# Optimization experiments

Hardware: AMD Instinct MI355X
Metric: run time of the kernel (lower is better)

Reference implementation:

```python
import jax, jax.numpy as jnp
import numpy as np

B, S, H = 2, 2048, 2048
NH = 16
Q_LORA = 1536
KV_LORA = 512
NOPE = 128
ROPE = 64
QHD = NOPE + ROPE  # 192
VHD = 128
FF = 8192
EPS = 1e-6
THETA = 10000.0


def rmsnorm(x, w, eps=EPS):
    var = jnp.mean(jnp.square(x), axis=-1, keepdims=True)
    return w * (x * jax.lax.rsqrt(var + eps))


def rotate_half(x):
    x1 = x[..., : x.shape[-1] // 2]
    x2 = x[..., x.shape[-1] // 2 :]
    return jnp.concatenate((-x2, x1), axis=-1)


def _deinterleave(x):
    # torch: x.view(b,h,s,d//2,2).transpose(0,1,2,4,3).reshape(b,h,s,d)
    b, h, s, d = x.shape
    return x.reshape(b, h, s, d // 2, 2).transpose(0, 1, 2, 4, 3).reshape(b, h, s, d)


def setup_inputs() -> dict:
    key = jax.random.key(0)
    ks = jax.random.split(key, 16)
    sc = 0.02
    # RoPE tables [S, ROPE]
    inv_freq = 1.0 / (THETA ** (np.arange(0, ROPE, 2, dtype=np.float64) / ROPE))
    freqs = np.outer(np.arange(S, dtype=np.float64), inv_freq)
    emb = np.concatenate([freqs, freqs], axis=-1)
    pos = jnp.sort(jax.random.randint(ks[15], (B, S), 0, S), axis=-1)
    return {
        "hidden_states": jax.random.normal(ks[0], (B, S, H), jnp.float32),
        "ln1_w": jnp.ones((H,), jnp.float32),
        "q_a_kernel": jax.random.normal(ks[1], (H, Q_LORA), jnp.float32) * sc,
        "q_a_ln_w": jnp.ones((Q_LORA,), jnp.float32),
        "q_b_kernel": jax.random.normal(ks[2], (Q_LORA, NH * QHD), jnp.float32) * sc,
        "kv_a_kernel": jax.random.normal(ks[3], (H, KV_LORA + ROPE), jnp.float32) * sc,
        "kv_a_ln_w": jnp.ones((KV_LORA,), jnp.float32),
        "kv_b_kernel": jax.random.normal(ks[4], (KV_LORA, NH * (NOPE + VHD)), jnp.float32) * sc,
        "o_kernel": jax.random.normal(ks[5], (NH * VHD, H), jnp.float32) * sc,
        "ln2_w": jnp.ones((H,), jnp.float32),
        "gate_kernel": jax.random.normal(ks[6], (H, FF), jnp.float32) * sc,
        "up_kernel": jax.random.normal(ks[7], (H, FF), jnp.float32) * sc,
        "down_kernel": jax.random.normal(ks[8], (FF, H), jnp.float32) * sc,
        "sin": jnp.asarray(np.sin(emb), jnp.float32),
        "cos": jnp.asarray(np.cos(emb), jnp.float32),
        "position_ids": pos,
    }


def reference(hidden_states, ln1_w, q_a_kernel, q_a_ln_w, q_b_kernel,
              kv_a_kernel, kv_a_ln_w, kv_b_kernel, o_kernel, ln2_w,
              gate_kernel, up_kernel, down_kernel, sin, cos, position_ids):
    b, s, h = hidden_states.shape
    x = rmsnorm(hidden_states, ln1_w)

    # --- MLA attention ---
    q = rmsnorm(x @ q_a_kernel, q_a_ln_w) @ q_b_kernel        # [b,s,NH*QHD]
    q = q.reshape(b, s, NH, QHD).transpose(0, 2, 1, 3)        # [b,NH,s,QHD]
    q_nope, q_pe = q[..., :NOPE], q[..., NOPE:]

    ckv = x @ kv_a_kernel                                     # [b,s,KV_LORA+ROPE]
    k_pe = ckv[..., KV_LORA:].reshape(b, s, 1, ROPE).transpose(0, 2, 1, 3)  # [b,1,s,ROPE]
    kv = rmsnorm(ckv[..., :KV_LORA], kv_a_ln_w) @ kv_b_kernel
    kv = kv.reshape(b, s, NH, NOPE + VHD).transpose(0, 2, 1, 3)
    k_nope = kv[..., :NOPE]
    v = kv[..., NOPE:]                                        # [b,NH,s,VHD]

    cos_e = cos[position_ids][:, None]                        # [b,1,s,ROPE]
    sin_e = sin[position_ids][:, None]
    q_pe = _deinterleave(q_pe)
    k_pe = _deinterleave(k_pe)
    q_pe = q_pe * cos_e + rotate_half(q_pe) * sin_e
    k_pe = k_pe * cos_e + rotate_half(k_pe) * sin_e

    qs = jnp.concatenate([q_nope, q_pe], axis=-1)             # [b,NH,s,QHD]
    ks = jnp.concatenate([k_nope, jnp.broadcast_to(k_pe, (b, NH, s, ROPE))], axis=-1)

    scale = QHD ** -0.5
    scores = jnp.einsum("bhqd,bhkd->bhqk", qs, ks) * scale
    causal = jnp.tril(jnp.ones((s, s), dtype=bool))
    scores = jnp.where(causal, scores, jnp.finfo(scores.dtype).min)
    probs = jax.nn.softmax(scores, axis=-1)
    attn = jnp.einsum("bhqk,bhkd->bhqd", probs, v)            # [b,NH,s,VHD]
    attn = attn.transpose(0, 2, 1, 3).reshape(b, s, NH * VHD)
    attn_out = attn @ o_kernel

    h1 = hidden_states + attn_out

    # --- dense MLP (SwiGLU) ---
    x2 = rmsnorm(h1, ln2_w)
    mlp = (jax.nn.silu(x2 @ gate_kernel) * (x2 @ up_kernel)) @ down_kernel
    return h1 + mlp
```

## Files before the change

kernel.cpp:

```cpp
#include <hip/hip_runtime.h>
#include <hip/hip_bf16.h>
#include <cstdint>

#define B_ 2
#define S_ 2048
#define H_ 2048
#define NH_ 16
#define QL_ 1536
#define KVL_ 512
#define NOPE_ 128
#define ROPE_ 64
#define QHD_ 192
#define VHD_ 128
#define FF_ 8192
#define BS_ (B_ * S_)
#define CKVP_ 640
#define KVW_ (NOPE_ + VHD_)

typedef __hip_bfloat16 bf16;
typedef __attribute__((ext_vector_type(8))) short short8_t;
typedef __attribute__((ext_vector_type(4))) float f32x4;

__device__ __forceinline__ float ldf(const float* p, size_t i) { return p[i]; }
__device__ __forceinline__ float ldf(const bf16* p, size_t i) { return __bfloat162float(p[i]); }
__device__ __forceinline__ void stf(float* p, size_t i, float v) { p[i] = v; }
__device__ __forceinline__ void stf(bf16* p, size_t i, float v) { p[i] = __float2bfloat16(v); }

__device__ __forceinline__ void gload16(const void* g, void* l)
{
    __builtin_amdgcn_global_load_lds((const unsigned int*)g, (unsigned int*)l, 16, 0, 0);
}

__global__ __launch_bounds__(256) void transp_bf16(
    const float* __restrict__ in, bf16* __restrict__ out, int K, int N, int Npad)
{
    __shared__ float t[32][33];
    const int n0 = blockIdx.x * 32, k0 = blockIdx.y * 32;
    for (int r = threadIdx.y; r < 32; r += 8) {
        const int n = n0 + threadIdx.x;
        t[r][threadIdx.x] = (n < N) ? in[(size_t)(k0 + r) * N + n] : 0.f;
    }
    __syncthreads();
    for (int r = threadIdx.y; r < 32; r += 8) {
        out[(size_t)(n0 + r) * K + k0 + threadIdx.x] = __float2bfloat16(t[threadIdx.x][r]);
    }
}

template<typename InT, typename OutT>
__global__ __launch_bounds__(256) void rmsnorm2(
    const InT* __restrict__ in, const float* __restrict__ w,
    OutT* __restrict__ out, int cols, int istride, int ostride)
{
    const int row = blockIdx.x;
    const InT* ip = in + (size_t)row * istride;
    OutT* op = out + (size_t)row * ostride;

    float ss = 0.f;
    for (int c = threadIdx.x; c < cols; c += 256) {
        float v = ldf(ip, c);
        ss = fmaf(v, v, ss);
    }
    #pragma unroll
    for (int off = 32; off; off >>= 1) ss += __shfl_xor(ss, off);
    __shared__ float red[4];
    if ((threadIdx.x & 63) == 0) red[threadIdx.x >> 6] = ss;
    __syncthreads();
    const float total = red[0] + red[1] + red[2] + red[3];
    const float scale = rsqrtf(total / (float)cols + 1e-6f);
    for (int c = threadIdx.x; c < cols; c += 256) {
        stf(op, c, ldf(ip, c) * scale * w[c]);
    }
}

template<int MODE, typename OutT>
__global__ __launch_bounds__(256) void gemm_bf16(
    const bf16* __restrict__ A, const bf16* __restrict__ BT,
    const float* __restrict__ Df, const bf16* __restrict__ Db,
    OutT* __restrict__ C, int M, int N, int K)
{
    __shared__ short As[128 * 32];
    __shared__ short Bs[128 * 32];
    const int tid = threadIdx.x;
    const int wid = tid >> 6, lane = tid & 63;
    const int bm = blockIdx.y * 128, bn = blockIdx.x * 128;
    const int wr = (wid >> 1) * 64, wc = (wid & 1) * 64;
    const int l16 = lane & 15;
    const int lk = (lane >> 4) << 3;

    f32x4 acc[4][4] = {};

    for (int k0 = 0; k0 < K; k0 += 32) {
        #pragma unroll
        for (int is = 0; is < 2; ++is) {
            const int c = is * 256 + tid;
            const int row = c >> 2;
            const int cb = (c & 3) * 16;
            const char* srcA = (const char*)A + ((size_t)(bm + row) * K + k0) * 2 + cb;
            const char* srcB = (const char*)BT + ((size_t)(bn + row) * K + k0) * 2 + cb;
            char* dstA = (char*)As + (is * 256 + wid * 64) * 16;
            char* dstB = (char*)Bs + (is * 256 + wid * 64) * 16;
            gload16(srcA, dstA);
            gload16(srcB, dstB);
        }
        __syncthreads();

        short8_t a[4], b[4];
        const short* ApW = As + (wr + l16) * 32 + lk;
        const short* BpW = Bs + (wc + l16) * 32 + lk;
        #pragma unroll
        for (int m = 0; m < 4; ++m) a[m] = *(const short8_t*)(ApW + m * 16 * 32);
        #pragma unroll
        for (int n = 0; n < 4; ++n) b[n] = *(const short8_t*)(BpW + n * 16 * 32);
        #pragma unroll
        for (int m = 0; m < 4; ++m)
            #pragma unroll
            for (int n = 0; n < 4; ++n)
                acc[m][n] = __builtin_amdgcn_mfma_f32_16x16x32_bf16(a[m], b[n], acc[m][n], 0, 0, 0);
        __syncthreads();
    }

    const int r0 = bm + wr + ((lane >> 4) << 2);
    const int c0 = bn + wc + l16;
    #pragma unroll
    for (int m = 0; m < 4; ++m) {
        #pragma unroll
        for (int n = 0; n < 4; ++n) {
            const int row = r0 + m * 16;
            const int col = c0 + n * 16;
            #pragma unroll
            for (int r = 0; r < 4; ++r) {
                const size_t off = (size_t)(row + r) * N + col;
                float v = acc[m][n][r];
                if (MODE == 1) v += Df[off];
                if (MODE == 2) {
                    const float g = __bfloat162float(Db[off]);
                    v *= g / (1.f + __expf(-g));
                }
                stf(C, off, v);
            }
        }
    }
}

__device__ __forceinline__ short8_t ldsfrag(const short* half_base, int r, int c)
{
    return *(const short8_t*)(half_base + r * 64 + ((c ^ (r & 7)) << 3));
}

template<int MODE, typename OutT>
__global__ __launch_bounds__(512, 2) void gemm256(
    const bf16* __restrict__ A, const bf16* __restrict__ BT,
    const float* __restrict__ Df, const bf16* __restrict__ Db,
    OutT* __restrict__ C, int M, int N, int K)
{
    __shared__ short lds[2][2][2][128 * 64];

    const int tid = threadIdx.x;
    const int wid = tid >> 6, lane = tid & 63;
    const int wm = wid >> 2, wn = wid & 3;
    const int l16 = lane & 15, hk = lane >> 4;

    const int nwg = gridDim.x * gridDim.y;
    const int orig = blockIdx.y * gridDim.x + blockIdx.x;
    const int q = nwg >> 3, r8 = nwg & 7;
    const int xcd = orig & 7, lid = orig >> 3;
    const int wg = (xcd < r8 ? xcd * (q + 1) : r8 * (q + 1) + (xcd - r8) * q) + lid;
    const int bn = (wg % gridDim.x) * 256;
    const int bm = (wg / gridDim.x) * 256;

    f32x4 acc[8][4] = {};

    const int nt = K >> 6;

    auto stage_half = [&](const bf16* gbase, int ldk, short* lbase) {
        #pragma unroll
        for (int i = 0; i < 2; ++i) {
            const int ch = i * 512 + tid;
            const int row = ch >> 3, pc = ch & 7;
            const int gc = pc ^ (row & 7);
            const char* src = (const char*)(gbase + (size_t)row * ldk + gc * 8);
            char* dst = (char*)lbase + (i * 512 + wid * 64) * 16;
            gload16(src, dst);
        }
    };

    stage_half(A + (size_t)bm * K, K, &lds[0][0][0][0]);
    stage_half(A + (size_t)(bm + 128) * K, K, &lds[0][0][1][0]);
    stage_half(BT + (size_t)bn * K, K, &lds[0][1][0][0]);
    stage_half(BT + (size_t)(bn + 128) * K, K, &lds[0][1][1][0]);
    asm volatile("s_waitcnt vmcnt(0)" ::: "memory");
    __syncthreads();

    int cur = 0;
    for (int t = 0; t < nt; ++t) {
        const int k0n = (t + 1) << 6;
        const short* Ah = &lds[cur][0][wm][0];
        const short* Bh = &lds[cur][1][wn >> 1][0];
        const int brr = (wn & 1) * 64;

        short8_t bfr[4][2], afr[2][2];

        #pragma unroll
        for (int nf = 0; nf < 4; ++nf)
            #pragma unroll
            for (int ks = 0; ks < 2; ++ks)
                bfr[nf][ks] = ldsfrag(Bh, brr + nf * 16 + l16, ks * 4 + hk);
        #pragma unroll
        for (int mi = 0; mi < 2; ++mi)
            #pragma unroll
            for (int ks = 0; ks < 2; ++ks)
                afr[mi][ks] = ldsfrag(Ah, mi * 16 + l16, ks * 4 + hk);
        if (t + 1 < nt) {
            stage_half(A + (size_t)bm * K + k0n, K, &lds[cur ^ 1][0][0][0]);
            stage_half(A + (size_t)(bm + 128) * K + k0n, K, &lds[cur ^ 1][0][1][0]);
        }
        __builtin_amdgcn_s_barrier();
        __builtin_amdgcn_s_setprio(1);
        #pragma unroll
        for (int mi = 0; mi < 2; ++mi)
            #pragma unroll
            for (int nf = 0; nf < 4; ++nf)
                #pragma unroll
                for (int ks = 0; ks < 2; ++ks)
                    acc[mi][nf] = __builtin_amdgcn_mfma_f32_16x16x32_bf16(
                        afr[mi][ks], bfr[nf][ks], acc[mi][nf], 0, 0, 0);
        __builtin_amdgcn_s_setprio(0);
        __builtin_amdgcn_s_barrier();

        #pragma unroll
        for (int mi = 0; mi < 2; ++mi)
            #pragma unroll
            for (int ks = 0; ks < 2; ++ks)
                afr[mi][ks] = ldsfrag(Ah, 32 + mi * 16 + l16, ks * 4 + hk);
        if (t + 1 < nt) {
            stage_half(BT + (size_t)bn * K + k0n, K, &lds[cur ^ 1][1][0][0]);
            stage_half(BT + (size_t)(bn + 128) * K + k0n, K, &lds[cur ^ 1][1][1][0]);
        }
        __builtin_amdgcn_s_barrier();
        __builtin_amdgcn_s_setprio(1);
        #pragma unroll
        for (int mi = 0; mi < 2; ++mi)
            #pragma unroll
            for (int nf = 0; nf < 4; ++nf)
                #pragma unroll
                for (int ks = 0; ks < 2; ++ks)
                    acc[2 + mi][nf] = __builtin_amdgcn_mfma_f32_16x16x32_bf16(
                        afr[mi][ks], bfr[nf][ks], acc[2 + mi][nf], 0, 0, 0);
        __builtin_amdgcn_s_setprio(0);
        __builtin_amdgcn_s_barrier();

        #pragma unroll
        for (int mi = 0; mi < 2; ++mi)
            #pragma unroll
            for (int ks = 0; ks < 2; ++ks)
                afr[mi][ks] = ldsfrag(Ah, 64 + mi * 16 + l16, ks * 4 + hk);
        __builtin_amdgcn_s_barrier();
        __builtin_amdgcn_s_setprio(1);
        #pragma unroll
        for (int mi = 0; mi < 2; ++mi)
            #pragma unroll
            for (int nf = 0; nf < 4; ++nf)
                #pragma unroll
                for (int ks = 0; ks < 2; ++ks)
                    acc[4 + mi][nf] = __builtin_amdgcn_mfma_f32_16x16x32_bf16(
                        afr[mi][ks], bfr[nf][ks], acc[4 + mi][nf], 0, 0, 0);
        __builtin_amdgcn_s_setprio(0);
        __builtin_amdgcn_s_barrier();

        #pragma unroll
        for (int mi = 0; mi < 2; ++mi)
            #pragma unroll
            for (int ks = 0; ks < 2; ++ks)
                afr[mi][ks] = ldsfrag(Ah, 96 + mi * 16 + l16, ks * 4 + hk);
        __builtin_amdgcn_s_barrier();
        __builtin_amdgcn_s_setprio(1);
        #pragma unroll
        for (int mi = 0; mi < 2; ++mi)
            #pragma unroll
            for (int nf = 0; nf < 4; ++nf)
                #pragma unroll
                for (int ks = 0; ks < 2; ++ks)
                    acc[6 + mi][nf] = __builtin_amdgcn_mfma_f32_16x16x32_bf16(
                        afr[mi][ks], bfr[nf][ks], acc[6 + mi][nf], 0, 0, 0);
        __builtin_amdgcn_s_setprio(0);
        asm volatile("s_waitcnt vmcnt(0)" ::: "memory");
        __syncthreads();
        cur ^= 1;
    }

    const int r0 = bm + wm * 128 + (lane >> 4) * 4;
    const int c0 = bn + wn * 64 + l16;
    #pragma unroll
    for (int mf = 0; mf < 8; ++mf) {
        #pragma unroll
        for (int nf = 0; nf < 4; ++nf) {
            const int row = r0 + mf * 16;
            const int col = c0 + nf * 16;
            #pragma unroll
            for (int r = 0; r < 4; ++r) {
                const size_t off = (size_t)(row + r) * N + col;
                float v = acc[mf][nf][r];
                if (MODE == 1) v += Df[off];
                if (MODE == 2) {
                    const float g = __bfloat162float(Db[off]);
                    v *= g / (1.f + __expf(-g));
                }
                stf(C, off, v);
            }
        }
    }
}

__global__ __launch_bounds__(256) void rope_kernel(
    bf16* __restrict__ q, float* __restrict__ ckv,
    const int* __restrict__ pos_ids,
    const float* __restrict__ sinT, const float* __restrict__ cosT)
{
    const int wid = blockIdx.x * 4 + (threadIdx.x >> 6);
    const int lane = threadIdx.x & 63;
    const int NQ = BS_ * NH_;

    int bs;
    bf16* bptr = nullptr;
    float* fptr = nullptr;
    if (wid < NQ) {
        bs = wid >> 4;
        bptr = q + (size_t)wid * QHD_ + NOPE_;
    } else {
        bs = wid - NQ;
        fptr = ckv + (size_t)bs * CKVP_ + KVL_;
    }
    const int pos = pos_ids[bs];
    const float c  = cosT[pos * ROPE_ + lane];
    const float sn = sinT[pos * ROPE_ + lane];
    const float x = bptr ? __bfloat162float(bptr[lane]) : fptr[lane];
    const int j = lane & 31;
    const float x0 = __shfl(x, 2 * j);
    const float x1 = __shfl(x, 2 * j + 1);
    const float res = (lane < 32) ? fmaf(x0, c, -x1 * sn) : fmaf(x1, c, x0 * sn);
    if (bptr) bptr[lane] = __float2bfloat16(res);
    else      fptr[lane] = res;
}

__global__ __launch_bounds__(256) void pack_k(
    const float* __restrict__ KV, const float* __restrict__ CKV,
    bf16* __restrict__ Kh)
{
    const int total = BS_ * NH_ * (QHD_ / 2);
    for (int i = blockIdx.x * 256 + threadIdx.x; i < total; i += gridDim.x * 256) {
        const int d2 = i % (QHD_ / 2);
        const int t  = i / (QHD_ / 2);
        const int s  = t % S_;
        const int hh = (t / S_) % NH_;
        const int bb = t / (S_ * NH_);
        const int d = d2 * 2;
        float2 v;
        if (d < NOPE_) v = *(const float2*)&KV[(((size_t)bb * S_ + s) * NH_ + hh) * KVW_ + d];
        else           v = *(const float2*)&CKV[((size_t)bb * S_ + s) * CKVP_ + KVL_ + (d - NOPE_)];
        union { bf16 h[2]; unsigned int u; } cv;
        cv.h[0] = __float2bfloat16(v.x);
        cv.h[1] = __float2bfloat16(v.y);
        *(unsigned int*)&Kh[((size_t)(bb * NH_ + hh) * S_ + s) * QHD_ + d] = cv.u;
    }
}

__global__ __launch_bounds__(256) void pack_vt(
    const float* __restrict__ KV, bf16* __restrict__ Vt)
{
    __shared__ float t[32][33];
    const int s0 = blockIdx.x * 32, d0 = blockIdx.y * 32;
    const int bh = blockIdx.z;
    const int tx = threadIdx.x & 31, ty = threadIdx.x >> 5;
    for (int r = ty; r < 32; r += 8)
        t[r][tx] = KV[(((size_t)(bh >> 4) * S_ + s0 + r) * NH_ + (bh & 15)) * KVW_ + NOPE_ + d0 + tx];
    __syncthreads();
    for (int r = ty; r < 32; r += 8)
        Vt[((size_t)bh * VHD_ + d0 + r) * S_ + s0 + tx] = __float2bfloat16(t[tx][r]);
}

__global__ __launch_bounds__(512, 2) void attn_mfma(
    const bf16* __restrict__ Qp, const bf16* __restrict__ Kh,
    const bf16* __restrict__ Vt, bf16* __restrict__ outp)
{
    __shared__ __align__(16) short Ks[64][192];
    __shared__ __align__(16) short Vs[128][64];
    __shared__ __align__(16) short Ps[8][16][64];

    const int tid = threadIdx.x;
    const int wid = tid >> 6, lane = tid & 63;
    const int l16 = lane & 15;
    const int hk  = lane >> 4;
    const int lk  = hk << 3;
    const int pr  = hk << 2;
    const int lx  = l16 & 7;

    const int bid = blockIdx.x;
    const int orig = (bid & 7) * 64 + (bid >> 3);
    const int j  = orig & 15;
    const int gh = orig >> 4;
    const int h = gh & 15, b = gh >> 4;

    const int setB = wid >> 2;
    const int qblk = setB ? (31 - j) : j;
    const int qw = qblk * 64 + (wid & 3) * 16;
    const int myNt = qblk + 1;
    const int ntStage = 32 - j;

    short8_t qf[6];
    const bf16* qbase = Qp + (((size_t)b * S_ + qw + l16) * NH_ + h) * QHD_;
    #pragma unroll
    for (int kk = 0; kk < 6; ++kk)
        qf[kk] = *(const short8_t*)(qbase + kk * 32 + lk);

    const bf16* Khb = Kh + (size_t)(b * NH_ + h) * S_ * QHD_;
    const bf16* Vtb = Vt + (size_t)(b * NH_ + h) * VHD_ * S_;

    f32x4 o[8] = {};
    float mr[4] = {-3.0e38f, -3.0e38f, -3.0e38f, -3.0e38f};
    float lr[4] = {0.f, 0.f, 0.f, 0.f};
    const float scale = 0.07216878364870323f;

    const int krow = tid >> 3, kc0 = (tid & 7) * 3;
    const int vrow = tid >> 2, vc0 = (tid & 3) * 2;

    short8_t kreg[3], vreg[2];
    auto load_tile = [&](int kt) {
        const short* ksrc = (const short*)(Khb + ((size_t)(kt * 64 + krow)) * QHD_);
        kreg[0] = *(const short8_t*)(ksrc + (kc0 + 0) * 8);
        kreg[1] = *(const short8_t*)(ksrc + (kc0 + 1) * 8);
        kreg[2] = *(const short8_t*)(ksrc + (kc0 + 2) * 8);
        const short* vsrc = (const short*)(Vtb + (size_t)vrow * S_ + kt * 64);
        vreg[0] = *(const short8_t*)(vsrc + (vc0 + 0) * 8);
        vreg[1] = *(const short8_t*)(vsrc + (vc0 + 1) * 8);
    };
    auto write_tile = [&]() {
        const int kx = krow & 7, vx = vrow & 7;
        *(short8_t*)&Ks[krow][((kc0 + 0) ^ kx) << 3] = kreg[0];
        *(short8_t*)&Ks[krow][((kc0 + 1) ^ kx) << 3] = kreg[1];
        *(short8_t*)&Ks[krow][((kc0 + 2) ^ kx) << 3] = kreg[2];
        *(short8_t*)&Vs[vrow][((vc0 + 0) ^ vx) << 3] = vreg[0];
        *(short8_t*)&Vs[vrow][((vc0 + 1) ^ vx) << 3] = vreg[1];
    };

    load_tile(0);

    for (int t = 0; t < ntStage; ++t) {
        write_tile();
        __syncthreads();
        if (t + 1 < ntStage) load_tile(t + 1);
        if (t < myNt) {
            const int k0 = t << 6;
            f32x4 s[4] = {};
            #pragma unroll
            for (int kk = 0; kk < 6; ++kk) {
                #pragma unroll
                for (int n = 0; n < 4; ++n) {
                    short8_t kf = *(const short8_t*)&Ks[n * 16 + l16][((kk * 4 + hk) ^ lx) << 3];
                    s[n] = __builtin_amdgcn_mfma_f32_16x16x32_bf16(qf[kk], kf, s[n], 0, 0, 0);
                }
            }
            if (t == myNt - 1) {
                #pragma unroll
                for (int n = 0; n < 4; ++n) {
                    const int kg = k0 + n * 16 + l16;
                    #pragma unroll
                    for (int r = 0; r < 4; ++r) {
                        if (kg > qw + pr + r) s[n][r] = -3.0e38f;
                    }
                }
            }
            #pragma unroll
            for (int r = 0; r < 4; ++r) {
                float rm = fmaxf(fmaxf(s[0][r], s[1][r]), fmaxf(s[2][r], s[3][r]));
                rm = fmaxf(rm, __shfl_xor(rm, 1));
                rm = fmaxf(rm, __shfl_xor(rm, 2));
                rm = fmaxf(rm, __shfl_xor(rm, 4));
                rm = fmaxf(rm, __shfl_xor(rm, 8));
                const float mnew = fmaxf(mr[r], rm);
                const float corr = __expf((mr[r] - mnew) * scale);
                mr[r] = mnew;
                float rs = 0.f;
                #pragma unroll
                for (int n = 0; n < 4; ++n) {
                    const float p = __expf((s[n][r] - mnew) * scale);
                    s[n][r] = p;
                    rs += p;
                }
                rs += __shfl_xor(rs, 1);
                rs += __shfl_xor(rs, 2);
                rs += __shfl_xor(rs, 4);
                rs += __shfl_xor(rs, 8);
                lr[r] = lr[r] * corr + rs;
                #pragma unroll
                for (int n = 0; n < 8; ++n) o[n][r] *= corr;
            }
            #pragma unroll
            for (int n = 0; n < 4; ++n) {
                #pragma unroll
                for (int r = 0; r < 4; ++r) {
                    union { bf16 hh; short u; } cv;
                    cv.hh = __float2bfloat16(s[n][r]);
                    const int row = pr + r;
                    const int col = (((n * 2 + (l16 >> 3)) ^ (row & 7)) << 3) + (l16 & 7);
                    Ps[wid][row][col] = cv.u;
                }
            }
            #pragma unroll
            for (int kk2 = 0; kk2 < 2; ++kk2) {
                short8_t pf = *(const short8_t*)&Ps[wid][l16][((kk2 * 4 + hk) ^ lx) << 3];
                #pragma unroll
                for (int n = 0; n < 8; ++n) {
                    short8_t vf = *(const short8_t*)&Vs[n * 16 + l16][((kk2 * 4 + hk) ^ lx) << 3];
                    o[n] = __builtin_amdgcn_mfma_f32_16x16x32_bf16(pf, vf, o[n], 0, 0, 0);
                }
            }
        }
        __syncthreads();
    }

    float inv[4];
    #pragma unroll
    for (int r = 0; r < 4; ++r) inv[r] = 1.f / lr[r];
    bf16* ob = outp + (((size_t)b * S_ + qw + pr) * NH_ + h) * VHD_;
    #pragma unroll
    for (int r = 0; r < 4; ++r)
        #pragma unroll
        for (int n = 0; n < 8; ++n)
            ob[(size_t)r * (NH_ * VHD_) + n * 16 + l16] = __float2bfloat16(o[n][r] * inv[r]);
}

extern "C" void kernel_launch(void* const* d_in, const int* in_sizes, int n_in,
                              void* d_out, int out_size, void* d_ws, size_t ws_size,
                              hipStream_t stream)
{
    const float* hidden  = (const float*)d_in[0];
    const float* ln1_w   = (const float*)d_in[1];
    const float* q_a_k   = (const float*)d_in[2];
    const float* q_a_ln  = (const float*)d_in[3];
    const float* q_b_k   = (const float*)d_in[4];
    const float* kv_a_k  = (const float*)d_in[5];
    const float* kv_a_ln = (const float*)d_in[6];
    const float* kv_b_k  = (const float*)d_in[7];
    const float* o_k     = (const float*)d_in[8];
    const float* ln2_w   = (const float*)d_in[9];
    const float* gate_k  = (const float*)d_in[10];
    const float* up_k    = (const float*)d_in[11];
    const float* down_k  = (const float*)d_in[12];
    const float* sinT    = (const float*)d_in[13];
    const float* cosT    = (const float*)d_in[14];
    const int*   pos     = (const int*)d_in[15];
    float* out = (float*)d_out;
    char* ws = (char*)d_ws;

    bf16* qaT   = (bf16*)(ws + 0);
    bf16* qbT   = (bf16*)(ws + 6291456);
    bf16* kvaT  = (bf16*)(ws + 15728640);
    bf16* kvbT  = (bf16*)(ws + 18350080);
    bf16* oT    = (bf16*)(ws + 22544384);
    bf16* Xb    = (bf16*)(ws + 30932992);
    bf16* QAb   = (bf16*)(ws + 47710208);
    bf16* CKVNb = (bf16*)(ws + 60293120);
    bf16* Qb    = (bf16*)(ws + 64487424);
    float* CKV  = (float*)(ws + 89653248);
    float* KV   = (float*)(ws + 100139008);
    bf16* ATTNb = (bf16*)(ws + 167247872);
    bf16* Vt    = (bf16*)(ws + 0);
    bf16* Kh    = (bf16*)(ws + 30932992);
    bf16* gateT = (bf16*)(ws + 0);
    bf16* upT   = (bf16*)(ws + 33554432);
    bf16* downT = (bf16*)(ws + 67108864);
    bf16* X2b   = (bf16*)(ws + 100663296);
    bf16* MLPb  = (bf16*)(ws + 117440512);

    const dim3 tb(32, 8);

    transp_bf16<<<dim3(1536 / 32, 2048 / 32), tb, 0, stream>>>(q_a_k, qaT, 2048, 1536, 1536);
    transp_bf16<<<dim3(3072 / 32, 1536 / 32), tb, 0, stream>>>(q_b_k, qbT, 1536, 3072, 3072);
    transp_bf16<<<dim3(640 / 32, 2048 / 32), tb, 0, stream>>>(kv_a_k, kvaT, 2048, 576, 640);
    transp_bf16<<<dim3(4096 / 32, 512 / 32), tb, 0, stream>>>(kv_b_k, kvbT, 512, 4096, 4096);
    transp_bf16<<<dim3(2048 / 32, 2048 / 32), tb, 0, stream>>>(o_k, oT, 2048, 2048, 2048);

    rmsnorm2<float, bf16><<<BS_, 256, 0, stream>>>(hidden, ln1_w, Xb, H_, H_, H_);
    gemm_bf16<0, bf16><<<dim3(QL_ / 128, BS_ / 128), 256, 0, stream>>>(
        Xb, qaT, nullptr, nullptr, QAb, BS_, QL_, H_);
    rmsnorm2<bf16, bf16><<<BS_, 256, 0, stream>>>(QAb, q_a_ln, QAb, QL_, QL_, QL_);
    gemm256<0, bf16><<<dim3((NH_ * QHD_) / 256, BS_ / 256), 512, 0, stream>>>(
        QAb, qbT, nullptr, nullptr, Qb, BS_, NH_ * QHD_, QL_);
    gemm_bf16<0, float><<<dim3(CKVP_ / 128, BS_ / 128), 256, 0, stream>>>(
        Xb, kvaT, nullptr, nullptr, CKV, BS_, CKVP_, H_);
    rmsnorm2<float, bf16><<<BS_, 256, 0, stream>>>(CKV, kv_a_ln, CKVNb, KVL_, CKVP_, KVL_);
    gemm256<0, float><<<dim3((NH_ * KVW_) / 256, BS_ / 256), 512, 0, stream>>>(
        CKVNb, kvbT, nullptr, nullptr, KV, BS_, NH_ * KVW_, KVL_);
    rope_kernel<<<(BS_ * NH_ + BS_) / 4, 256, 0, stream>>>(Qb, CKV, pos, sinT, cosT);
    pack_k<<<2048, 256, 0, stream>>>(KV, CKV, Kh);
    pack_vt<<<dim3(S_ / 32, VHD_ / 32, B_ * NH_), 256, 0, stream>>>(KV, Vt);
    attn_mfma<<<dim3(512), 512, 0, stream>>>(Qb, Kh, Vt, ATTNb);
    gemm256<1, float><<<dim3(H_ / 256, BS_ / 256), 512, 0, stream>>>(
        ATTNb, oT, hidden, nullptr, out, BS_, H_, NH_ * VHD_);

    transp_bf16<<<dim3(8192 / 32, 2048 / 32), tb, 0, stream>>>(gate_k, gateT, 2048, 8192, 8192);
    transp_bf16<<<dim3(8192 / 32, 2048 / 32), tb, 0, stream>>>(up_k, upT, 2048, 8192, 8192);
    transp_bf16<<<dim3(2048 / 32, 8192 / 32), tb, 0, stream>>>(down_k, downT, 8192, 2048, 2048);

    rmsnorm2<float, bf16><<<BS_, 256, 0, stream>>>(out, ln2_w, X2b, H_, H_, H_);
    gemm256<0, bf16><<<dim3(FF_ / 256, BS_ / 256), 512, 0, stream>>>(
        X2b, gateT, nullptr, nullptr, MLPb, BS_, FF_, H_);
    gemm256<2, bf16><<<dim3(FF_ / 256, BS_ / 256), 512, 0, stream>>>(
        X2b, upT, nullptr, MLPb, MLPb, BS_, FF_, H_);
    gemm256<1, float><<<dim3(H_ / 256, BS_ / 256), 512, 0, stream>>>(
        MLPb, downT, out, nullptr, out, BS_, H_, FF_);
}
```

Before: 1.071 ms.

## Rework GEMM pipeline to 4-stage ring, add 256x128 tile and fused gate/up GEMM

Replaces the double-buffered 64-deep K loop of the 256x256 GEMM with a 4-slot LDS ring of 32-deep K steps. Each step waits with a counted vmcnt and issues a single barrier, so loads are prefetched three steps ahead. Adds a 256x128 tile variant used for the q_a, q_b, o-proj and down projections, giving more workgroups for small-N shapes. Adds a dual-B kernel that computes gate and up together and applies SiLU-multiply in the epilogue, so the MLP intermediate is no longer written and re-read. The cost is a new LDS layout without XOR swizzle, which may cause bank conflicts, and more launches of smaller tiles with less operand reuse.

```diff
diff --git a/kernel.cpp b/kernel.cpp
--- a/kernel.cpp
+++ b/kernel.cpp
@@ -142,9 +142,23 @@
     }
 }
 
-__device__ __forceinline__ short8_t ldsfrag(const short* half_base, int r, int c)
-{
-    return *(const short8_t*)(half_base + r * 64 + ((c ^ (r & 7)) << 3));
+__device__ __forceinline__ short8_t ring_frag(const short* region, int row, int hk)
+{
+    return *(const short8_t*)(region + ((row >> 3) << 8) + (hk << 6) + ((row & 7) << 3));
+}
+
+template<int MODE, typename OutT>
+__device__ __forceinline__ void epi_store(
+    OutT* __restrict__ C, const float* __restrict__ Df, const bf16* __restrict__ Db,
+    int N, int row, int col, float v)
+{
+    const size_t off = (size_t)row * N + col;
+    if (MODE == 1) v += Df[off];
+    if (MODE == 2) {
+        const float g = __bfloat162float(Db[off]);
+        v *= g / (1.f + __expf(-g));
+    }
+    stf(C, off, v);
 }
 
 template<int MODE, typename OutT>
@@ -153,7 +167,7 @@
     const float* __restrict__ Df, const bf16* __restrict__ Db,
     OutT* __restrict__ C, int M, int N, int K)
 {
-    __shared__ short lds[2][2][2][128 * 64];
+    __shared__ short lds[4 * 16384];
 
     const int tid = threadIdx.x;
     const int wid = tid >> 6, lane = tid & 63;
@@ -169,146 +183,234 @@
     const int bm = (wg / gridDim.x) * 256;
 
     f32x4 acc[8][4] = {};
-
-    const int nt = K >> 6;
-
-    auto stage_half = [&](const bf16* gbase, int ldk, short* lbase) {
-        #pragma unroll
-        for (int i = 0; i < 2; ++i) {
-            const int ch = i * 512 + tid;
-            const int row = ch >> 3, pc = ch & 7;
-            const int gc = pc ^ (row & 7);
-            const char* src = (const char*)(gbase + (size_t)row * ldk + gc * 8);
-            char* dst = (char*)lbase + (i * 512 + wid * 64) * 16;
-            gload16(src, dst);
+    const int nt = K >> 5;
+
+    auto stage_step = [&](int s) {
+        short* base = &lds[(s & 3) * 16384];
+        const bf16* ga = A + (size_t)bm * K + s * 32;
+        const bf16* gb = BT + (size_t)bn * K + s * 32;
+        #pragma unroll
+        for (int j = 0; j < 2; ++j) {
+            const int i = j * 512 + tid;
+            const int row = ((i >> 5) << 3) | (i & 7);
+            const int ch = (i >> 3) & 3;
+            gload16(ga + (size_t)row * K + ch * 8, (char*)base + i * 16);
+            gload16(gb + (size_t)row * K + ch * 8, (char*)(base + 8192) + i * 16);
         }
     };
 
-    stage_half(A + (size_t)bm * K, K, &lds[0][0][0][0]);
-    stage_half(A + (size_t)(bm + 128) * K, K, &lds[0][0][1][0]);
-    stage_half(BT + (size_t)bn * K, K, &lds[0][1][0][0]);
-    stage_half(BT + (size_t)(bn + 128) * K, K, &lds[0][1][1][0]);
-    asm volatile("s_waitcnt vmcnt(0)" ::: "memory");
-    __syncthreads();
-
-    int cur = 0;
-    for (int t = 0; t < nt; ++t) {
-        const int k0n = (t + 1) << 6;
-        const short* Ah = &lds[cur][0][wm][0];
-        const short* Bh = &lds[cur][1][wn >> 1][0];
-        const int brr = (wn & 1) * 64;
-
-        short8_t bfr[4][2], afr[2][2];
-
-        #pragma unroll
-        for (int nf = 0; nf < 4; ++nf)
-            #pragma unroll
-            for (int ks = 0; ks < 2; ++ks)
-                bfr[nf][ks] = ldsfrag(Bh, brr + nf * 16 + l16, ks * 4 + hk);
-        #pragma unroll
-        for (int mi = 0; mi < 2; ++mi)
-            #pragma unroll
-            for (int ks = 0; ks < 2; ++ks)
-                afr[mi][ks] = ldsfrag(Ah, mi * 16 + l16, ks * 4 + hk);
-        if (t + 1 < nt) {
-            stage_half(A + (size_t)bm * K + k0n, K, &lds[cur ^ 1][0][0][0]);
-            stage_half(A + (size_t)(bm + 128) * K + k0n, K, &lds[cur ^ 1][0][1][0]);
-        }
+    stage_step(0); stage_step(1); stage_step(2);
+
+    for (int s = 0; s < nt; ++s) {
+        if (s + 2 < nt)      asm volatile("s_waitcnt vmcnt(8)" ::: "memory");
+        else if (s + 1 < nt) asm volatile("s_waitcnt vmcnt(4)" ::: "memory");
+        else                 asm volatile("s_waitcnt vmcnt(0)" ::: "memory");
         __builtin_amdgcn_s_barrier();
+
+        const short* As = &lds[(s & 3) * 16384];
+        const short* Bs = As + 8192;
+        short8_t a[8], b[4];
+        #pragma unroll
+        for (int mf = 0; mf < 8; ++mf) a[mf] = ring_frag(As, wm * 128 + mf * 16 + l16, hk);
+        #pragma unroll
+        for (int nf = 0; nf < 4; ++nf) b[nf] = ring_frag(Bs, wn * 64 + nf * 16 + l16, hk);
+
+        if (s + 3 < nt) stage_step(s + 3);
+
         __builtin_amdgcn_s_setprio(1);
         #pragma unroll
-        for (int mi = 0; mi < 2; ++mi)
+        for (int mf = 0; mf < 8; ++mf)
             #pragma unroll
             for (int nf = 0; nf < 4; ++nf)
-                #pragma unroll
-                for (int ks = 0; ks < 2; ++ks)
-                    acc[mi][nf] = __builtin_amdgcn_mfma_f32_16x16x32_bf16(
-                        afr[mi][ks], bfr[nf][ks], acc[mi][nf], 0, 0, 0);
+                acc[mf][nf] = __builtin_amdgcn_mfma_f32_16x16x32_bf16(
+                    a[mf], b[nf], acc[mf][nf], 0, 0, 0);
         __builtin_amdgcn_s_setprio(0);
-        __builtin_amdgcn_s_barrier();
-
-        #pragma unroll
-        for (int mi = 0; mi < 2; ++mi)
-            #pragma unroll
-            for (int ks = 0; ks < 2; ++ks)
-                afr[mi][ks] = ldsfrag(Ah, 32 + mi * 16 + l16, ks * 4 + hk);
-        if (t + 1 < nt) {
-            stage_half(BT + (size_t)bn * K + k0n, K, &lds[cur ^ 1][1][0][0]);
-            stage_half(BT + (size_t)(bn + 128) * K + k0n, K, &lds[cur ^ 1][1][1][0]);
-        }
-        __builtin_amdgcn_s_barrier();
-        __builtin_amdgcn_s_setprio(1);
-        #pragma unroll
-        for (int mi = 0; mi < 2; ++mi)
-            #pragma unroll
-            for (int nf = 0; nf < 4; ++nf)
-                #pragma unroll
-                for (int ks = 0; ks < 2; ++ks)
-                    acc[2 + mi][nf] = __builtin_amdgcn_mfma_f32_16x16x32_bf16(
-                        afr[mi][ks], bfr[nf][ks], acc[2 + mi][nf], 0, 0, 0);
-        __builtin_amdgcn_s_setprio(0);
-        __builtin_amdgcn_s_barrier();
-
-        #pragma unroll
-        for (int mi = 0; mi < 2; ++mi)
-            #pragma unroll
-            for (int ks = 0; ks < 2; ++ks)
-                afr[mi][ks] = ldsfrag(Ah, 64 + mi * 16 + l16, ks * 4 + hk);
-        __builtin_amdgcn_s_barrier();
-        __builtin_amdgcn_s_setprio(1);
-        #pragma unroll
-        for (int mi = 0; mi < 2; ++mi)
-            #pragma unroll
-            for (int nf = 0; nf < 4; ++nf)
-                #pragma unroll
-                for (int ks = 0; ks < 2; ++ks)
-                    acc[4 + mi][nf] = __builtin_amdgcn_mfma_f32_16x16x32_bf16(
-                        afr[mi][ks], bfr[nf][ks], acc[4 + mi][nf], 0, 0, 0);
-        __builtin_amdgcn_s_setprio(0);
-        __builtin_amdgcn_s_barrier();
-
-        #pragma unroll
-        for (int mi = 0; mi < 2; ++mi)
-            #pragma unroll
-            for (int ks = 0; ks < 2; ++ks)
-                afr[mi][ks] = ldsfrag(Ah, 96 + mi * 16 + l16, ks * 4 + hk);
-        __builtin_amdgcn_s_barrier();
-        __builtin_amdgcn_s_setprio(1);
-        #pragma unroll
-        for (int mi = 0; mi < 2; ++mi)
-            #pragma unroll
-            for (int nf = 0; nf < 4; ++nf)
-                #pragma unroll
-                for (int ks = 0; ks < 2; ++ks)
-                    acc[6 + mi][nf] = __builtin_amdgcn_mfma_f32_16x16x32_bf16(
-                        afr[mi][ks], bfr[nf][ks], acc[6 + mi][nf], 0, 0, 0);
-        __builtin_amdgcn_s_setprio(0);
-        asm volatile("s_waitcnt vmcnt(0)" ::: "memory");
-        __syncthreads();
-        cur ^= 1;
     }
 
     const int r0 = bm + wm * 128 + (lane >> 4) * 4;
     const int c0 = bn + wn * 64 + l16;
     #pragma unroll
-    for (int mf = 0; mf < 8; ++mf) {
+    for (int mf = 0; mf < 8; ++mf)
+        #pragma unroll
+        for (int nf = 0; nf < 4; ++nf)
+            #pragma unroll
+            for (int r = 0; r < 4; ++r)
+                epi_store<MODE>(C, Df, Db, N, r0 + mf * 16 + r, c0 + nf * 16, acc[mf][nf][r]);
+}
+
+template<int MODE, typename OutT>
+__global__ __launch_bounds__(512, 2) void gemm256n128(
+    const bf16* __restrict__ A, const bf16* __restrict__ BT,
+    const float* __restrict__ Df, const bf16* __restrict__ Db,
+    OutT* __restrict__ C, int M, int N, int K)
+{
+    __shared__ short lds[4 * 12288];
+
+    const int tid = threadIdx.x;
+    const int wid = tid >> 6, lane = tid & 63;
+    const int wm = wid >> 1, wn = wid & 1;
+    const int l16 = lane & 15, hk = lane >> 4;
+
+    const int nwg = gridDim.x * gridDim.y;
+    const int orig = blockIdx.y * gridDim.x + blockIdx.x;
+    const int q = nwg >> 3, r8 = nwg & 7;
+    const int xcd = orig & 7, lid = orig >> 3;
+    const int wg = (xcd < r8 ? xcd * (q + 1) : r8 * (q + 1) + (xcd - r8) * q) + lid;
+    const int bn = (wg % gridDim.x) * 128;
+    const int bm = (wg / gridDim.x) * 256;
+
+    f32x4 acc[4][4] = {};
+    const int nt = K >> 5;
+
+    auto stage_step = [&](int s) {
+        short* base = &lds[(s & 3) * 12288];
+        const bf16* ga = A + (size_t)bm * K + s * 32;
+        const bf16* gb = BT + (size_t)bn * K + s * 32;
+        #pragma unroll
+        for (int j = 0; j < 2; ++j) {
+            const int i = j * 512 + tid;
+            const int row = ((i >> 5) << 3) | (i & 7);
+            const int ch = (i >> 3) & 3;
+            gload16(ga + (size_t)row * K + ch * 8, (char*)base + i * 16);
+        }
+        {
+            const int i = tid;
+            const int row = ((i >> 5) << 3) | (i & 7);
+            const int ch = (i >> 3) & 3;
+            gload16(gb + (size_t)row * K + ch * 8, (char*)(base + 8192) + i * 16);
+        }
+    };
+
+    stage_step(0); stage_step(1); stage_step(2);
+
+    for (int s = 0; s < nt; ++s) {
+        if (s + 2 < nt)      asm volatile("s_waitcnt vmcnt(6)" ::: "memory");
+        else if (s + 1 < nt) asm volatile("s_waitcnt vmcnt(3)" ::: "memory");
+        else                 asm volatile("s_waitcnt vmcnt(0)" ::: "memory");
+        __builtin_amdgcn_s_barrier();
+
+        const short* As = &lds[(s & 3) * 12288];
+        const short* Bs = As + 8192;
+        short8_t a[4], b[4];
+        #pragma unroll
+        for (int mf = 0; mf < 4; ++mf) a[mf] = ring_frag(As, wm * 64 + mf * 16 + l16, hk);
+        #pragma unroll
+        for (int nf = 0; nf < 4; ++nf) b[nf] = ring_frag(Bs, wn * 64 + nf * 16 + l16, hk);
+
+        if (s + 3 < nt) stage_step(s + 3);
+
+        __builtin_amdgcn_s_setprio(1);
+        #pragma unroll
+        for (int mf = 0; mf < 4; ++mf)
+            #pragma unroll
+            for (int nf = 0; nf < 4; ++nf)
+                acc[mf][nf] = __builtin_amdgcn_mfma_f32_16x16x32_bf16(
+                    a[mf], b[nf], acc[mf][nf], 0, 0, 0);
+        __builtin_amdgcn_s_setprio(0);
+    }
+
+    const int r0 = bm + wm * 64 + (lane >> 4) * 4;
+    const int c0 = bn + wn * 64 + l16;
+    #pragma unroll
+    for (int mf = 0; mf < 4; ++mf)
+        #pragma unroll
+        for (int nf = 0; nf < 4; ++nf)
+            #pragma unroll
+            for (int r = 0; r < 4; ++r)
+                epi_store<MODE>(C, Df, Db, N, r0 + mf * 16 + r, c0 + nf * 16, acc[mf][nf][r]);
+}
+
+__global__ __launch_bounds__(512, 2) void gemm256dual(
+    const bf16* __restrict__ A, const bf16* __restrict__ BG,
+    const bf16* __restrict__ BU, bf16* __restrict__ C, int M, int N, int K)
+{
+    __shared__ short lds[4 * 16384];
+
+    const int tid = threadIdx.x;
+    const int wid = tid >> 6, lane = tid & 63;
+    const int wm = wid >> 1, wn = wid & 1;
+    const int l16 = lane & 15, hk = lane >> 4;
+
+    const int nwg = gridDim.x * gridDim.y;
+    const int orig = blockIdx.y * gridDim.x + blockIdx.x;
+    const int q = nwg >> 3, r8 = nwg & 7;
+    const int xcd = orig & 7, lid = orig >> 3;
+    const int wg = (xcd < r8 ? xcd * (q + 1) : r8 * (q + 1) + (xcd - r8) * q) + lid;
+    const int bm = (wg % gridDim.y) * 256;
+    const int bn = (wg / gridDim.y) * 128;
+
+    f32x4 ag[4][4] = {}, au[4][4] = {};
+    const int nt = K >> 5;
+
+    auto stage_step = [&](int s) {
+        short* base = &lds[(s & 3) * 16384];
+        const bf16* ga = A + (size_t)bm * K + s * 32;
+        const bf16* gg = BG + (size_t)bn * K + s * 32;
+        const bf16* gu = BU + (size_t)bn * K + s * 32;
+        #pragma unroll
+        for (int j = 0; j < 2; ++j) {
+            const int i = j * 512 + tid;
+            const int row = ((i >> 5) << 3) | (i & 7);
+            const int ch = (i >> 3) & 3;
+            gload16(ga + (size_t)row * K + ch * 8, (char*)base + i * 16);
+        }
+        {
+            const int i = tid;
+            const int row = ((i >> 5) << 3) | (i & 7);
+            const int ch = (i >> 3) & 3;
+            gload16(gg + (size_t)row * K + ch * 8, (char*)(base + 8192) + i * 16);
+            gload16(gu + (size_t)row * K + ch * 8, (char*)(base + 12288) + i * 16);
+        }
+    };
+
+    stage_step(0); stage_step(1); stage_step(2);
+
+    for (int s = 0; s < nt; ++s) {
+        if (s + 2 < nt)      asm volatile("s_waitcnt vmcnt(8)" ::: "memory");
+        else if (s + 1 < nt) asm volatile("s_waitcnt vmcnt(4)" ::: "memory");
+        else                 asm volatile("s_waitcnt vmcnt(0)" ::: "memory");
+        __builtin_amdgcn_s_barrier();
+
+        const short* As = &lds[(s & 3) * 16384];
+        const short* Gs = As + 8192;
+        const short* Us = As + 12288;
+        short8_t a[4], g[4], u[4];
+        #pragma unroll
+        for (int mf = 0; mf < 4; ++mf) a[mf] = ring_frag(As, wm * 64 + mf * 16 + l16, hk);
         #pragma unroll
         for (int nf = 0; nf < 4; ++nf) {
-            const int row = r0 + mf * 16;
-            const int col = c0 + nf * 16;
+            g[nf] = ring_frag(Gs, wn * 64 + nf * 16 + l16, hk);
+            u[nf] = ring_frag(Us, wn * 64 + nf * 16 + l16, hk);
+        }
+
+        if (s + 3 < nt) stage_step(s + 3);
+
+        __builtin_amdgcn_s_setprio(1);
+        #pragma unroll
+        for (int mf = 0; mf < 4; ++mf)
+            #pragma unroll
+            for (int nf = 0; nf < 4; ++nf) {
+                ag[mf][nf] = __builtin_amdgcn_mfma_f32_16x16x32_bf16(
+                    a[mf], g[nf], ag[mf][nf], 0, 0, 0);
+                au[mf][nf] = __builtin_amdgcn_mfma_f32_16x16x32_bf16(
+                    a[mf], u[nf], au[mf][nf], 0, 0, 0);
+            }
+        __builtin_amdgcn_s_setprio(0);
+    }
+
+    const int r0 = bm + wm * 64 + (lane >> 4) * 4;
+    const int c0 = bn + wn * 64 + l16;
+    #pragma unroll
+    for (int mf = 0; mf < 4; ++mf)
+        #pragma unroll
+        for (int nf = 0; nf < 4; ++nf)
             #pragma unroll
             for (int r = 0; r < 4; ++r) {
-                const size_t off = (size_t)(row + r) * N + col;
-                float v = acc[mf][nf][r];
-                if (MODE == 1) v += Df[off];
-                if (MODE == 2) {
-                    const float g = __bfloat162float(Db[off]);
-                    v *= g / (1.f + __expf(-g));
-                }
-                stf(C, off, v);
+                const float gg = ag[mf][nf][r];
+                const float uu = au[mf][nf][r];
+                const float v = gg / (1.f + __expf(-gg)) * uu;
+                C[(size_t)(r0 + mf * 16 + r) * N + c0 + nf * 16] = __float2bfloat16(v);
             }
-        }
-    }
 }
 
 __global__ __launch_bounds__(256) void rope_kernel(
@@ -581,10 +683,10 @@
     transp_bf16<<<dim3(2048 / 32, 2048 / 32), tb, 0, stream>>>(o_k, oT, 2048, 2048, 2048);
 
     rmsnorm2<float, bf16><<<BS_, 256, 0, stream>>>(hidden, ln1_w, Xb, H_, H_, H_);
-    gemm_bf16<0, bf16><<<dim3(QL_ / 128, BS_ / 128), 256, 0, stream>>>(
+    gemm256n128<0, bf16><<<dim3(QL_ / 128, BS_ / 256), 512, 0, stream>>>(
         Xb, qaT, nullptr, nullptr, QAb, BS_, QL_, H_);
     rmsnorm2<bf16, bf16><<<BS_, 256, 0, stream>>>(QAb, q_a_ln, QAb, QL_, QL_, QL_);
-    gemm256<0, bf16><<<dim3((NH_ * QHD_) / 256, BS_ / 256), 512, 0, stream>>>(
+    gemm256n128<0, bf16><<<dim3((NH_ * QHD_) / 128, BS_ / 256), 512, 0, stream>>>(
         QAb, qbT, nullptr, nullptr, Qb, BS_, NH_ * QHD_, QL_);
     gemm_bf16<0, float><<<dim3(CKVP_ / 128, BS_ / 128), 256, 0, stream>>>(
         Xb, kvaT, nullptr, nullptr, CKV, BS_, CKVP_, H_);
@@ -595,7 +697,7 @@
     pack_k<<<2048, 256, 0, stream>>>(KV, CKV, Kh);
     pack_vt<<<dim3(S_ / 32, VHD_ / 32, B_ * NH_), 256, 0, stream>>>(KV, Vt);
     attn_mfma<<<dim3(512), 512, 0, stream>>>(Qb, Kh, Vt, ATTNb);
-    gemm256<1, float><<<dim3(H_ / 256, BS_ / 256), 512, 0, stream>>>(
+    gemm256n128<1, float><<<dim3(H_ / 128, BS_ / 256), 512, 0, stream>>>(
         ATTNb, oT, hidden, nullptr, out, BS_, H_, NH_ * VHD_);
 
     transp_bf16<<<dim3(8192 / 32, 2048 / 32), tb, 0, stream>>>(gate_k, gateT, 2048, 8192, 8192);
@@ -603,10 +705,8 @@
     transp_bf16<<<dim3(2048 / 32, 8192 / 32), tb, 0, stream>>>(down_k, downT, 8192, 2048, 2048);
 
     rmsnorm2<float, bf16><<<BS_, 256, 0, stream>>>(out, ln2_w, X2b, H_, H_, H_);
-    gemm256<0, bf16><<<dim3(FF_ / 256, BS_ / 256), 512, 0, stream>>>(
-        X2b, gateT, nullptr, nullptr, MLPb, BS_, FF_, H_);
-    gemm256<2, bf16><<<dim3(FF_ / 256, BS_ / 256), 512, 0, stream>>>(
-        X2b, upT, nullptr, MLPb, MLPb, BS_, FF_, H_);
-    gemm256<1, float><<<dim3(H_ / 256, BS_ / 256), 512, 0, stream>>>(
+    gemm256dual<<<dim3(FF_ / 128, BS_ / 256), 512, 0, stream>>>(
+        X2b, gateT, upT, MLPb, BS_, FF_, H_);
+    gemm256n128<1, float><<<dim3(H_ / 128, BS_ / 256), 512, 0, stream>>>(
         MLPb, downT, out, nullptr, out, BS_, H_, FF_);
 }
```

Result: no change. 1.085 ms (+1.3%).
